# Performance work log

Hardware: AMD Instinct MI355X
Metric: run time of the kernel (lower is better)

Reference implementation:

```python
import jax, jax.numpy as jnp
import numpy as np

B, T, C, H, HS, L, V, BITS = 4, 512, 768, 12, 64, 12, 50257, 16


def _ln(x, g, b, eps=1e-5):
    m = x.mean(-1, keepdims=True)
    v = ((x - m) ** 2).mean(-1, keepdims=True)
    return (x - m) * jax.lax.rsqrt(v + eps) * g + b


def setup_inputs() -> dict:
    key = jax.random.key(0)
    ks = jax.random.split(key, 12)
    s = 0.02
    return {
        "idx": jax.random.randint(ks[0], (B, T), 0, V),
        "tok_emb": jax.random.normal(ks[1], (V, C), jnp.float32) * s,
        "pos_emb": jax.random.normal(ks[2], (T, C), jnp.float32) * s,
        "Wq": jax.random.normal(ks[3], (L, H, C, HS), jnp.float32) * s,
        "Wk": jax.random.normal(ks[4], (L, H, C, HS), jnp.float32) * s,
        "Wv": jax.random.normal(ks[5], (L, H, C, HS), jnp.float32) * s,
        "Wo": jax.random.normal(ks[6], (L, C, C), jnp.float32) * s,
        "bo": jnp.zeros((L, C), jnp.float32),
        "W1": jax.random.normal(ks[7], (L, C, 4 * C), jnp.float32) * s,
        "b1": jnp.zeros((L, 4 * C), jnp.float32),
        "W2": jax.random.normal(ks[8], (L, 4 * C, C), jnp.float32) * s,
        "b2": jnp.zeros((L, C), jnp.float32),
        "ln1_g": jnp.ones((L, C), jnp.float32),
        "ln1_b": jnp.zeros((L, C), jnp.float32),
        "ln2_g": jnp.ones((L, C), jnp.float32),
        "ln2_b": jnp.zeros((L, C), jnp.float32),
        "lnf_g": jnp.ones((C,), jnp.float32),
        "lnf_b": jnp.zeros((C,), jnp.float32),
        "Wh": jax.random.normal(ks[9], (C, BITS), jnp.float32) * s,
        "bh": jnp.zeros((BITS,), jnp.float32),
    }


def reference(idx, tok_emb, pos_emb, Wq, Wk, Wv, Wo, bo, W1, b1, W2, b2,
              ln1_g, ln1_b, ln2_g, ln2_b, lnf_g, lnf_b, Wh, bh):
    Bc, Tc = idx.shape
    x = tok_emb[idx] + pos_emb[:Tc]          # [B,T,C]
    mask = jnp.tril(jnp.ones((Tc, Tc), bool))  # causal tril buffer
    scale = HS ** -0.5

    def block(x, p):
        wq, wk, wv, wo, bo_, w1, b1_, w2, b2_, g1, bb1, g2, bb2 = p
        xn = _ln(x, g1, bb1)
        q = jnp.einsum('btc,hcd->bhtd', xn, wq)
        k = jnp.einsum('btc,hcd->bhtd', xn, wk)
        v = jnp.einsum('btc,hcd->bhtd', xn, wv)
        wei = jnp.einsum('bhtd,bhsd->bhts', q, k) * scale
        wei = jnp.where(mask, wei, -jnp.inf)
        wei = jax.nn.softmax(wei, axis=-1)
        o = jnp.einsum('bhts,bhsd->bhtd', wei, v)
        o = o.transpose(0, 2, 1, 3).reshape(Bc, Tc, H * HS)  # concat heads
        x = x + o @ wo + bo_
        xn2 = _ln(x, g2, bb2)
        h = jax.nn.gelu(xn2 @ w1 + b1_, approximate=False)  # exact GELU (torch default)
        x = x + h @ w2 + b2_
        return x, None

    x, _ = jax.lax.scan(block, x, (Wq, Wk, Wv, Wo, bo, W1, b1, W2, b2,
                                   ln1_g, ln1_b, ln2_g, ln2_b))
    x = _ln(x, lnf_g, lnf_b)
    logits = x @ Wh + bh                      # [B,T,16] ECOC logits
    return logits
```

## Files before the change

kernel.cpp:

```cpp
#include <hip/hip_runtime.h>
#include <hip/hip_bf16.h>
#include <math.h>

#define TT   512
#define CC   768
#define HH   12
#define HSZ  64
#define LL   12
#define C4   3072
#define BTOT 2048
#define NQKV 2304
#define NX   ((long)BTOT * CC)

typedef __attribute__((ext_vector_type(8))) short short8;
typedef __attribute__((ext_vector_type(4))) float f32x4;

__device__ __forceinline__ unsigned short f2b_bits(float f) {
    unsigned u = __float_as_uint(f);
    return (unsigned short)((u + 0x7fffu + ((u >> 16) & 1u)) >> 16);
}

__device__ __forceinline__ void gl_lds16(const void* g, void* l) {
    __builtin_amdgcn_global_load_lds(
        (const __attribute__((address_space(1))) unsigned int*)g,
        (__attribute__((address_space(3))) unsigned int*)l,
        16, 0, 0);
}

__global__ __launch_bounds__(256) void embed_k(const int* __restrict__ idx,
    const float* __restrict__ tok, const float* __restrict__ pos,
    float* __restrict__ x)
{
    int r   = blockIdx.x;
    int tid = threadIdx.x;
    int t   = r & (TT - 1);
    long id = idx[r];
    const float* te = tok + id * (long)CC;
    const float* pe = pos + (long)t * CC;
    float* xr = x + (long)r * CC;
#pragma unroll
    for (int i = 0; i < 3; ++i) {
        int c = tid + i * 256;
        xr[c] = te[c] + pe[c];
    }
}

__global__ __launch_bounds__(256) void ln_b(const float* __restrict__ x,
    const float* __restrict__ g, const float* __restrict__ b,
    __hip_bfloat16* __restrict__ y)
{
    int r = blockIdx.x, tid = threadIdx.x;
    const float* xr = x + (long)r * CC;
    float v[3];
    v[0] = xr[tid]; v[1] = xr[tid + 256]; v[2] = xr[tid + 512];
    float s  = v[0] + v[1] + v[2];
    float sq = v[0]*v[0] + v[1]*v[1] + v[2]*v[2];
#pragma unroll
    for (int off = 32; off > 0; off >>= 1) {
        s  += __shfl_down(s, off);
        sq += __shfl_down(sq, off);
    }
    __shared__ float ss[4], ssq[4];
    int w = tid >> 6;
    if ((tid & 63) == 0) { ss[w] = s; ssq[w] = sq; }
    __syncthreads();
    s  = ss[0] + ss[1] + ss[2] + ss[3];
    sq = ssq[0] + ssq[1] + ssq[2] + ssq[3];
    float mean = s * (1.0f / CC);
    float var  = sq * (1.0f / CC) - mean * mean;
    float rs   = rsqrtf(var + 1e-5f);
    __hip_bfloat16* yr = y + (long)r * CC;
#pragma unroll
    for (int i = 0; i < 3; ++i) {
        int c = tid + i * 256;
        yr[c] = __float2bfloat16((v[i] - mean) * rs * g[c] + b[c]);
    }
}

template <bool DOLN>
__global__ __launch_bounds__(256) void red_ln(float* __restrict__ x,
    const float* __restrict__ p, const float* __restrict__ bias,
    const float* __restrict__ g, const float* __restrict__ b,
    __hip_bfloat16* __restrict__ y)
{
    int r = blockIdx.x, tid = threadIdx.x;
    float* xr = x + (long)r * CC;
    const float* pr = p + (long)r * CC;
    float v[3];
#pragma unroll
    for (int i = 0; i < 3; ++i) {
        int c = tid + i * 256;
        float s = xr[c] + bias[c];
        s += pr[c];
        s += pr[c + 1 * NX];
        s += pr[c + 2 * NX];
        s += pr[c + 3 * NX];
        xr[c] = s;
        v[i] = s;
    }
    if (!DOLN) return;
    float s  = v[0] + v[1] + v[2];
    float sq = v[0]*v[0] + v[1]*v[1] + v[2]*v[2];
#pragma unroll
    for (int off = 32; off > 0; off >>= 1) {
        s  += __shfl_down(s, off);
        sq += __shfl_down(sq, off);
    }
    __shared__ float ss[4], ssq[4];
    int w = tid >> 6;
    if ((tid & 63) == 0) { ss[w] = s; ssq[w] = sq; }
    __syncthreads();
    s  = ss[0] + ss[1] + ss[2] + ss[3];
    sq = ssq[0] + ssq[1] + ssq[2] + ssq[3];
    float mean = s * (1.0f / CC);
    float var  = sq * (1.0f / CC) - mean * mean;
    float rs   = rsqrtf(var + 1e-5f);
    __hip_bfloat16* yr = y + (long)r * CC;
#pragma unroll
    for (int i = 0; i < 3; ++i) {
        int c = tid + i * 256;
        yr[c] = __float2bfloat16((v[i] - mean) * rs * g[c] + b[c]);
    }
}

__global__ __launch_bounds__(256) void cvtT_k(const float* __restrict__ src,
    __hip_bfloat16* __restrict__ dst, int R, int D, long sSrc, long sDst)
{
    src += (long)blockIdx.z * sSrc;
    dst += (long)blockIdx.z * sDst;
    __shared__ float t[64][65];
    int d0 = blockIdx.x * 64, r0 = blockIdx.y * 64;
    int tid = threadIdx.x;
#pragma unroll
    for (int i = 0; i < 4; ++i) {
        int flat = tid + i * 256;
        int r = flat >> 4, c4 = (flat & 15) * 4;
        float4 v = *(const float4*)&src[(long)(r0 + r) * D + d0 + c4];
        t[r][c4 + 0] = v.x; t[r][c4 + 1] = v.y;
        t[r][c4 + 2] = v.z; t[r][c4 + 3] = v.w;
    }
    __syncthreads();
#pragma unroll
    for (int i = 0; i < 4; ++i) {
        int flat = tid + i * 256;
        int n = flat >> 4, kq = (flat & 15) * 4;
        ushort4 o;
        o.x = f2b_bits(t[kq + 0][n]); o.y = f2b_bits(t[kq + 1][n]);
        o.z = f2b_bits(t[kq + 2][n]); o.w = f2b_bits(t[kq + 3][n]);
        *(ushort4*)&dst[(long)(d0 + n) * R + r0 + kq] = o;
    }
}

__global__ __launch_bounds__(256) void cvt_qkvT(const float* __restrict__ Wq,
    const float* __restrict__ Wk, const float* __restrict__ Wv,
    __hip_bfloat16* __restrict__ out)
{
    int c0 = blockIdx.x * 64;
    int g  = blockIdx.y;
    int l  = blockIdx.z;
    int which = g / 12, h = g % 12;
    const long wAtt = (long)HH * CC * HSZ;
    const float* src = (which == 0 ? Wq : which == 1 ? Wk : Wv)
                       + l * wAtt + (long)h * CC * HSZ;
    __hip_bfloat16* dst = out + (long)l * NQKV * CC + (long)(which * CC + h * HSZ) * CC;
    __shared__ float t[64][65];
    int tid = threadIdx.x;
#pragma unroll
    for (int i = 0; i < 4; ++i) {
        int flat = tid + i * 256;
        int r = flat >> 4, c4 = (flat & 15) * 4;
        float4 v = *(const float4*)&src[(long)(c0 + r) * HSZ + c4];
        t[r][c4 + 0] = v.x; t[r][c4 + 1] = v.y;
        t[r][c4 + 2] = v.z; t[r][c4 + 3] = v.w;
    }
    __syncthreads();
#pragma unroll
    for (int i = 0; i < 4; ++i) {
        int flat = tid + i * 256;
        int n = flat >> 4, kq = (flat & 15) * 4;
        ushort4 o;
        o.x = f2b_bits(t[kq + 0][n]); o.y = f2b_bits(t[kq + 1][n]);
        o.z = f2b_bits(t[kq + 2][n]); o.w = f2b_bits(t[kq + 3][n]);
        *(ushort4*)&dst[(long)n * CC + c0 + kq] = o;
    }
}

template <int EPI>
__global__ __launch_bounds__(256, 3) void gemm_bf16(
    const __hip_bfloat16* __restrict__ A,
    const __hip_bfloat16* __restrict__ BT,
    __hip_bfloat16* __restrict__ Cb, float* __restrict__ Cf,
    const float* __restrict__ bias, __hip_bfloat16* __restrict__ Vt,
    int K, int lda, int ldb, int ldc)
{
    __shared__ short Asm[4][64 * 32];
    __shared__ short Bsm[4][128 * 32];
    const int tid  = threadIdx.x;
    const int lane = tid & 63;
    const int wid  = tid >> 6;
    const int wm = wid >> 1, wn = wid & 1;
    const int row0 = blockIdx.y * 64, col0 = blockIdx.x * 128;
    const int sk = (EPI == 5) ? blockIdx.z : 0;

    const int gr = tid >> 2;
    const int cb = ((tid & 3) + (tid >> 3)) & 3;
    const int gk = cb * 8;
    const __hip_bfloat16* Ap = A  + (long)(row0 + gr) * lda + sk * K + gk;
    const __hip_bfloat16* Bp = BT + (long)(col0 + gr) * ldb + sk * K + gk;
    const int lofs = wid * 512;

    f32x4 acc[2][4] = {};
    const int fr = lane & 15, g = lane >> 4;

    int offA[2], offB[4];
#pragma unroll
    for (int m = 0; m < 2; ++m) {
        int row = wm * 32 + m * 16 + fr;
        offA[m] = row * 32 + (((g - (row >> 1)) & 3) * 8);
    }
#pragma unroll
    for (int n = 0; n < 4; ++n) {
        int row = wn * 64 + n * 16 + fr;
        offB[n] = row * 32 + (((g - (row >> 1)) & 3) * 8);
    }

#define STAGE(buf)                                                          \
    do {                                                                    \
        gl_lds16(Ap, &Asm[buf][lofs]);                                      \
        gl_lds16(Bp, &Bsm[buf][lofs]);                                      \
        gl_lds16(Bp + (long)64 * ldb, &Bsm[buf][lofs + 64 * 32]);           \
        Ap += 32; Bp += 32;                                                 \
    } while (0)

    STAGE(0); STAGE(1); STAGE(2);

    const int nt = K >> 5;
    for (int t = 0; t < nt; ++t) {
        if (t < nt - 2)       asm volatile("s_waitcnt vmcnt(6)" ::: "memory");
        else if (t == nt - 2) asm volatile("s_waitcnt vmcnt(3)" ::: "memory");
        else                  asm volatile("s_waitcnt vmcnt(0)" ::: "memory");
        __builtin_amdgcn_s_barrier();
        __builtin_amdgcn_sched_barrier(0);
        if (t + 3 < nt) STAGE((t + 3) & 3);

        const int cur = t & 3;
        short8 af[2], bf[4];
#pragma unroll
        for (int m = 0; m < 2; ++m)
            af[m] = *(const short8*)&Asm[cur][offA[m]];
#pragma unroll
        for (int n = 0; n < 4; ++n)
            bf[n] = *(const short8*)&Bsm[cur][offB[n]];
#pragma unroll
        for (int m = 0; m < 2; ++m)
#pragma unroll
            for (int n = 0; n < 4; ++n)
                acc[m][n] = __builtin_amdgcn_mfma_f32_16x16x32_bf16(
                    af[m], bf[n], acc[m][n], 0, 0, 0);
    }
#undef STAGE

    const int fq = lane >> 4;
    float* pout = (EPI == 5) ? (Cf + (long)sk * NX) : nullptr;
#pragma unroll
    for (int m = 0; m < 2; ++m) {
        int rbase = row0 + wm * 32 + m * 16 + fq * 4;
#pragma unroll
        for (int n = 0; n < 4; ++n) {
            int col = col0 + wn * 64 + n * 16 + fr;
            if (EPI == 1 && col >= 1536) {
                int hd = col - 1536;
                int b = rbase >> 9, t = rbase & (TT - 1);
                ushort4 o;
                o.x = f2b_bits(acc[m][n][0]); o.y = f2b_bits(acc[m][n][1]);
                o.z = f2b_bits(acc[m][n][2]); o.w = f2b_bits(acc[m][n][3]);
                *(ushort4*)&Vt[((long)(b * HH + (hd >> 6)) * HSZ + (hd & 63)) * TT + t] = o;
                continue;
            }
            float bv = (EPI == 2) ? bias[col] : 0.f;
#pragma unroll
            for (int j = 0; j < 4; ++j) {
                long row = rbase + j;
                float v = acc[m][n][j];
                if (EPI == 1) {
                    Cb[row * ldc + col] = __float2bfloat16(v);
                } else if (EPI == 2) {
                    v += bv;
                    v = 0.5f * v * (1.0f + erff(v * 0.70710678118654752f));
                    Cb[row * ldc + col] = __float2bfloat16(v);
                } else {
                    pout[row * ldc + col] = v;
                }
            }
        }
    }
}

__global__ __launch_bounds__(64) void attn_mfma(
    const __hip_bfloat16* __restrict__ qkv,
    const __hip_bfloat16* __restrict__ vT,
    __hip_bfloat16* __restrict__ o)
{
    const int qt = blockIdx.x;
    const int h  = blockIdx.y;
    const int b  = blockIdx.z;
    const int lane = threadIdx.x;
    const int t0 = qt * 16;
    const int fr = lane & 15, g = lane >> 4;

    __shared__ unsigned short P_lds[16 * 40];
    __shared__ float corr_lds[16], l_lds[16];

    const long qbase = ((long)(b * TT + t0 + fr)) * NQKV + h * HSZ + g * 8;
    short8 qf0 = *(const short8*)(qkv + qbase);
    short8 qf1 = *(const short8*)(qkv + qbase + 32);

    f32x4 oacc[4] = {};
    float m_run = -3.0e38f, l_run = 0.f;
    const int t_lane = t0 + fr;
    const int smax = t0 + 15;
    const long kcol = CC + h * HSZ + g * 8;
    const long vrow = (((long)(b * HH + h) * HSZ) + fr) * TT + g * 8;

    short8 ka0, ka1, ka2, ka3;
    {
        long kb0 = ((long)(b * TT + fr)) * NQKV + kcol;
        long kb1 = ((long)(b * TT + 16 + fr)) * NQKV + kcol;
        ka0 = *(const short8*)(qkv + kb0);
        ka1 = *(const short8*)(qkv + kb0 + 32);
        ka2 = *(const short8*)(qkv + kb1);
        ka3 = *(const short8*)(qkv + kb1 + 32);
    }

    for (int s0 = 0; s0 <= smax; s0 += 32) {
        f32x4 st0 = {}, st1 = {};
        st0 = __builtin_amdgcn_mfma_f32_16x16x32_bf16(ka0, qf0, st0, 0, 0, 0);
        st0 = __builtin_amdgcn_mfma_f32_16x16x32_bf16(ka1, qf1, st0, 0, 0, 0);
        st1 = __builtin_amdgcn_mfma_f32_16x16x32_bf16(ka2, qf0, st1, 0, 0, 0);
        st1 = __builtin_amdgcn_mfma_f32_16x16x32_bf16(ka3, qf1, st1, 0, 0, 0);

        const bool more = (s0 + 32 <= smax);
        short8 kn0, kn1, kn2, kn3;
        if (more) {
            long kb0 = ((long)(b * TT + s0 + 32 + fr)) * NQKV + kcol;
            long kb1 = ((long)(b * TT + s0 + 48 + fr)) * NQKV + kcol;
            kn0 = *(const short8*)(qkv + kb0);
            kn1 = *(const short8*)(qkv + kb0 + 32);
            kn2 = *(const short8*)(qkv + kb1);
            kn3 = *(const short8*)(qkv + kb1 + 32);
        }
        short8 vc0 = *(const short8*)(vT + vrow + s0);
        short8 vc1 = *(const short8*)(vT + vrow + 16 * TT + s0);
        short8 vc2 = *(const short8*)(vT + vrow + 32 * TT + s0);
        short8 vc3 = *(const short8*)(vT + vrow + 48 * TT + s0);

        float p[8];
        float mx = -3.0e38f;
#pragma unroll
        for (int j = 0; j < 4; ++j) {
            int s = s0 + g * 4 + j;
            float v = st0[j] * 0.125f;
            v = (s <= t_lane) ? v : -3.0e38f;
            p[j] = v; mx = fmaxf(mx, v);
        }
#pragma unroll
        for (int j = 0; j < 4; ++j) {
            int s = s0 + 16 + g * 4 + j;
            float v = st1[j] * 0.125f;
            v = (s <= t_lane) ? v : -3.0e38f;
            p[4 + j] = v; mx = fmaxf(mx, v);
        }
        mx = fmaxf(mx, __shfl_xor(mx, 16));
        mx = fmaxf(mx, __shfl_xor(mx, 32));
        float mnew = fmaxf(m_run, mx);
        float corr = __expf(m_run - mnew);
        float psum = 0.f;
#pragma unroll
        for (int i = 0; i < 8; ++i) {
            float e = __expf(p[i] - mnew);
            p[i] = e; psum += e;
        }
        psum += __shfl_xor(psum, 16);
        psum += __shfl_xor(psum, 32);
        l_run = l_run * corr + psum;
        m_run = mnew;

        __syncthreads();
        if (lane < 16) corr_lds[lane] = corr;
        unsigned u0 = (unsigned)f2b_bits(p[0]) | ((unsigned)f2b_bits(p[1]) << 16);
        unsigned u1 = (unsigned)f2b_bits(p[2]) | ((unsigned)f2b_bits(p[3]) << 16);
        unsigned u2 = (unsigned)f2b_bits(p[4]) | ((unsigned)f2b_bits(p[5]) << 16);
        unsigned u3 = (unsigned)f2b_bits(p[6]) | ((unsigned)f2b_bits(p[7]) << 16);
        *(unsigned*)&P_lds[fr * 40 + g * 4]          = u0;
        *(unsigned*)&P_lds[fr * 40 + g * 4 + 2]      = u1;
        *(unsigned*)&P_lds[fr * 40 + 16 + g * 4]     = u2;
        *(unsigned*)&P_lds[fr * 40 + 16 + g * 4 + 2] = u3;
        __syncthreads();

        float cr0 = corr_lds[g * 4 + 0], cr1 = corr_lds[g * 4 + 1];
        float cr2 = corr_lds[g * 4 + 2], cr3 = corr_lds[g * 4 + 3];
        short8 pf = *(const short8*)&P_lds[fr * 40 + g * 8];
        oacc[0][0] *= cr0; oacc[0][1] *= cr1; oacc[0][2] *= cr2; oacc[0][3] *= cr3;
        oacc[0] = __builtin_amdgcn_mfma_f32_16x16x32_bf16(pf, vc0, oacc[0], 0, 0, 0);
        oacc[1][0] *= cr0; oacc[1][1] *= cr1; oacc[1][2] *= cr2; oacc[1][3] *= cr3;
        oacc[1] = __builtin_amdgcn_mfma_f32_16x16x32_bf16(pf, vc1, oacc[1], 0, 0, 0);
        oacc[2][0] *= cr0; oacc[2][1] *= cr1; oacc[2][2] *= cr2; oacc[2][3] *= cr3;
        oacc[2] = __builtin_amdgcn_mfma_f32_16x16x32_bf16(pf, vc2, oacc[2], 0, 0, 0);
        oacc[3][0] *= cr0; oacc[3][1] *= cr1; oacc[3][2] *= cr2; oacc[3][3] *= cr3;
        oacc[3] = __builtin_amdgcn_mfma_f32_16x16x32_bf16(pf, vc3, oacc[3], 0, 0, 0);

        if (more) { ka0 = kn0; ka1 = kn1; ka2 = kn2; ka3 = kn3; }
    }

    __syncthreads();
    if (lane < 16) l_lds[lane] = l_run;
    __syncthreads();
    float il0 = 1.f / l_lds[g * 4 + 0], il1 = 1.f / l_lds[g * 4 + 1];
    float il2 = 1.f / l_lds[g * 4 + 2], il3 = 1.f / l_lds[g * 4 + 3];
#pragma unroll
    for (int dt = 0; dt < 4; ++dt) {
        long cbase = (long)(b * TT + t0) * CC + h * HSZ + dt * 16 + fr;
        o[cbase + (g * 4 + 0) * (long)CC] = __float2bfloat16(oacc[dt][0] * il0);
        o[cbase + (g * 4 + 1) * (long)CC] = __float2bfloat16(oacc[dt][1] * il1);
        o[cbase + (g * 4 + 2) * (long)CC] = __float2bfloat16(oacc[dt][2] * il2);
        o[cbase + (g * 4 + 3) * (long)CC] = __float2bfloat16(oacc[dt][3] * il3);
    }
}

__global__ __launch_bounds__(256) void head_k(const float* __restrict__ x,
    const float* __restrict__ g, const float* __restrict__ bb,
    const float* __restrict__ Wh, const float* __restrict__ bh,
    float* __restrict__ out)
{
    int r = blockIdx.x, tid = threadIdx.x;
    const float* xr = x + (long)r * CC;
    float v[3];
    v[0] = xr[tid]; v[1] = xr[tid + 256]; v[2] = xr[tid + 512];
    float s  = v[0] + v[1] + v[2];
    float sq = v[0]*v[0] + v[1]*v[1] + v[2]*v[2];
#pragma unroll
    for (int off = 32; off > 0; off >>= 1) {
        s  += __shfl_down(s, off);
        sq += __shfl_down(sq, off);
    }
    __shared__ float ss[4], ssq[4];
    int w = tid >> 6;
    if ((tid & 63) == 0) { ss[w] = s; ssq[w] = sq; }
    __syncthreads();
    s  = ss[0] + ss[1] + ss[2] + ss[3];
    sq = ssq[0] + ssq[1] + ssq[2] + ssq[3];
    float mean = s * (1.0f / CC);
    float var  = sq * (1.0f / CC) - mean * mean;
    float rs   = rsqrtf(var + 1e-5f);

    float acc[16];
#pragma unroll
    for (int j = 0; j < 16; ++j) acc[j] = 0.f;
#pragma unroll
    for (int i = 0; i < 3; ++i) {
        int c = tid + i * 256;
        float xnv = (v[i] - mean) * rs * g[c] + bb[c];
        const float* wr = Wh + (long)c * 16;
#pragma unroll
        for (int j = 0; j < 16; ++j) acc[j] = fmaf(xnv, wr[j], acc[j]);
    }
#pragma unroll
    for (int off = 32; off > 0; off >>= 1)
#pragma unroll
        for (int j = 0; j < 16; ++j) acc[j] += __shfl_down(acc[j], off);
    __shared__ float red[4][16];
    if ((tid & 63) == 0)
#pragma unroll
        for (int j = 0; j < 16; ++j) red[w][j] = acc[j];
    __syncthreads();
    if (tid < 16)
        out[(long)r * 16 + tid] =
            red[0][tid] + red[1][tid] + red[2][tid] + red[3][tid] + bh[tid];
}

extern "C" void kernel_launch(void* const* d_in, const int* in_sizes, int n_in,
                              void* d_out, int out_size, void* d_ws, size_t ws_size,
                              hipStream_t stream)
{
    const int*   idx  = (const int*)  d_in[0];
    const float* tok  = (const float*)d_in[1];
    const float* pos  = (const float*)d_in[2];
    const float* Wq   = (const float*)d_in[3];
    const float* Wk   = (const float*)d_in[4];
    const float* Wv   = (const float*)d_in[5];
    const float* Wo   = (const float*)d_in[6];
    const float* bo   = (const float*)d_in[7];
    const float* W1   = (const float*)d_in[8];
    const float* b1   = (const float*)d_in[9];
    const float* W2   = (const float*)d_in[10];
    const float* b2   = (const float*)d_in[11];
    const float* ln1g = (const float*)d_in[12];
    const float* ln1b = (const float*)d_in[13];
    const float* ln2g = (const float*)d_in[14];
    const float* ln2b = (const float*)d_in[15];
    const float* lnfg = (const float*)d_in[16];
    const float* lnfb = (const float*)d_in[17];
    const float* Wh   = (const float*)d_in[18];
    const float* bh   = (const float*)d_in[19];

    char* w = (char*)d_ws;
    float*          x     = (float*)w;          w += NX * 4;
    __hip_bfloat16* xn_b  = (__hip_bfloat16*)w; w += NX * 2;
    __hip_bfloat16* qkvb  = (__hip_bfloat16*)w; w += (long)BTOT * NQKV * 2;
    __hip_bfloat16* vT    = (__hip_bfloat16*)w; w += NX * 2;
    __hip_bfloat16* o_b   = (__hip_bfloat16*)w; w += NX * 2;
    __hip_bfloat16* hb    = (__hip_bfloat16*)w; w += (long)BTOT * C4 * 2;
    __hip_bfloat16* qkvT  = (__hip_bfloat16*)w; w += (long)LL * NQKV * CC * 2;
    __hip_bfloat16* woT   = (__hip_bfloat16*)w; w += (long)LL * CC * CC * 2;
    __hip_bfloat16* w1T   = (__hip_bfloat16*)w; w += (long)LL * C4 * CC * 2;
    __hip_bfloat16* w2T   = (__hip_bfloat16*)w; w += (long)LL * CC * C4 * 2;
    float*          pbuf  = (float*)w;          w += 4 * NX * 4;

    cvt_qkvT<<<dim3(12, 36, LL), 256, 0, stream>>>(Wq, Wk, Wv, qkvT);
    cvtT_k<<<dim3(12, 12, LL), 256, 0, stream>>>(Wo, woT, CC, CC,
        (long)CC * CC, (long)CC * CC);
    cvtT_k<<<dim3(48, 12, LL), 256, 0, stream>>>(W1, w1T, CC, C4,
        (long)CC * C4, (long)CC * C4);
    cvtT_k<<<dim3(12, 48, LL), 256, 0, stream>>>(W2, w2T, C4, CC,
        (long)C4 * CC, (long)C4 * CC);

    embed_k<<<BTOT, 256, 0, stream>>>(idx, tok, pos, x);
    ln_b<<<BTOT, 256, 0, stream>>>(x, ln1g, ln1b, xn_b);

    for (int l = 0; l < LL; ++l) {
        gemm_bf16<1><<<dim3(NQKV / 128, BTOT / 64), 256, 0, stream>>>(
            xn_b, qkvT + (long)l * NQKV * CC, qkvb, nullptr, nullptr, vT,
            CC, CC, CC, NQKV);

        attn_mfma<<<dim3(TT / 16, HH, 4), 64, 0, stream>>>(qkvb, vT, o_b);

        gemm_bf16<5><<<dim3(CC / 128, BTOT / 64, 4), 256, 0, stream>>>(
            o_b, woT + (long)l * CC * CC, nullptr, pbuf, nullptr, nullptr,
            192, CC, CC, CC);

        red_ln<true><<<BTOT, 256, 0, stream>>>(x, pbuf, bo + l * CC,
            ln2g + l * CC, ln2b + l * CC, xn_b);

        gemm_bf16<2><<<dim3(C4 / 128, BTOT / 64), 256, 0, stream>>>(
            xn_b, w1T + (long)l * C4 * CC, hb, nullptr, b1 + l * C4, nullptr,
            CC, CC, CC, C4);

        gemm_bf16<5><<<dim3(CC / 128, BTOT / 64, 4), 256, 0, stream>>>(
            hb, w2T + (long)l * CC * C4, nullptr, pbuf, nullptr, nullptr,
            768, C4, C4, CC);

        if (l < LL - 1) {
            red_ln<true><<<BTOT, 256, 0, stream>>>(x, pbuf, b2 + l * CC,
                ln1g + (l + 1) * CC, ln1b + (l + 1) * CC, xn_b);
        } else {
            red_ln<false><<<BTOT, 256, 0, stream>>>(x, pbuf, b2 + l * CC,
                nullptr, nullptr, nullptr);
        }
    }

    head_k<<<BTOT, 256, 0, stream>>>(x, lnfg, lnfb, Wh, bh, (float*)d_out);
}
```

Before: 1.552 ms.

## Fuse attention, output projection, residual add and LayerNorm into one kernel

```diff
diff --git a/kernel.cpp b/kernel.cpp
--- a/kernel.cpp
+++ b/kernel.cpp
@@ -296,20 +296,30 @@
     }
 }
 
-__global__ __launch_bounds__(64) void attn_mfma(
+__global__ __launch_bounds__(768) void attn_proj(
     const __hip_bfloat16* __restrict__ qkv,
     const __hip_bfloat16* __restrict__ vT,
-    __hip_bfloat16* __restrict__ o)
+    const __hip_bfloat16* __restrict__ woT,
+    const float* __restrict__ bo,
+    const float* __restrict__ g2, const float* __restrict__ bb2,
+    float* __restrict__ x, __hip_bfloat16* __restrict__ xn)
 {
     const int qt = blockIdx.x;
-    const int h  = blockIdx.y;
-    const int b  = blockIdx.z;
-    const int lane = threadIdx.x;
+    const int b  = blockIdx.y;
+    const int tid = threadIdx.x;
+    const int wid = tid >> 6;
+    const int lane = tid & 63;
+    const int h = wid;
     const int t0 = qt * 16;
     const int fr = lane & 15, g = lane >> 4;
 
-    __shared__ unsigned short P_lds[16 * 40];
-    __shared__ float corr_lds[16], l_lds[16];
+    __shared__ unsigned short o_lds[16][776];
+    __shared__ unsigned short P_all[12][16 * 40];
+    __shared__ float corr_all[12][16], l_all[12][16];
+    __shared__ float sum_w[12][16], sq_w[12][16];
+    __shared__ float mean_s[16], rs_s[16];
+
+    unsigned short* P_w = P_all[wid];
 
     const long qbase = ((long)(b * TT + t0 + fr)) * NQKV + h * HSZ + g * 8;
     short8 qf0 = *(const short8*)(qkv + qbase);
@@ -385,21 +395,20 @@
         l_run = l_run * corr + psum;
         m_run = mnew;
 
-        __syncthreads();
-        if (lane < 16) corr_lds[lane] = corr;
+        if (lane < 16) corr_all[wid][lane] = corr;
         unsigned u0 = (unsigned)f2b_bits(p[0]) | ((unsigned)f2b_bits(p[1]) << 16);
         unsigned u1 = (unsigned)f2b_bits(p[2]) | ((unsigned)f2b_bits(p[3]) << 16);
         unsigned u2 = (unsigned)f2b_bits(p[4]) | ((unsigned)f2b_bits(p[5]) << 16);
         unsigned u3 = (unsigned)f2b_bits(p[6]) | ((unsigned)f2b_bits(p[7]) << 16);
-        *(unsigned*)&P_lds[fr * 40 + g * 4]          = u0;
-        *(unsigned*)&P_lds[fr * 40 + g * 4 + 2]      = u1;
-        *(unsigned*)&P_lds[fr * 40 + 16 + g * 4]     = u2;
-        *(unsigned*)&P_lds[fr * 40 + 16 + g * 4 + 2] = u3;
-        __syncthreads();
-
-        float cr0 = corr_lds[g * 4 + 0], cr1 = corr_lds[g * 4 + 1];
-        float cr2 = corr_lds[g * 4 + 2], cr3 = corr_lds[g * 4 + 3];
-        short8 pf = *(const short8*)&P_lds[fr * 40 + g * 8];
+        *(unsigned*)&P_w[fr * 40 + g * 4]          = u0;
+        *(unsigned*)&P_w[fr * 40 + g * 4 + 2]      = u1;
+        *(unsigned*)&P_w[fr * 40 + 16 + g * 4]     = u2;
+        *(unsigned*)&P_w[fr * 40 + 16 + g * 4 + 2] = u3;
+        __builtin_amdgcn_sched_barrier(0);
+
+        float cr0 = corr_all[wid][g * 4 + 0], cr1 = corr_all[wid][g * 4 + 1];
+        float cr2 = corr_all[wid][g * 4 + 2], cr3 = corr_all[wid][g * 4 + 3];
+        short8 pf = *(const short8*)&P_w[fr * 40 + g * 8];
         oacc[0][0] *= cr0; oacc[0][1] *= cr1; oacc[0][2] *= cr2; oacc[0][3] *= cr3;
         oacc[0] = __builtin_amdgcn_mfma_f32_16x16x32_bf16(pf, vc0, oacc[0], 0, 0, 0);
         oacc[1][0] *= cr0; oacc[1][1] *= cr1; oacc[1][2] *= cr2; oacc[1][3] *= cr3;
@@ -412,18 +421,99 @@
         if (more) { ka0 = kn0; ka1 = kn1; ka2 = kn2; ka3 = kn3; }
     }
 
-    __syncthreads();
-    if (lane < 16) l_lds[lane] = l_run;
-    __syncthreads();
-    float il0 = 1.f / l_lds[g * 4 + 0], il1 = 1.f / l_lds[g * 4 + 1];
-    float il2 = 1.f / l_lds[g * 4 + 2], il3 = 1.f / l_lds[g * 4 + 3];
-#pragma unroll
-    for (int dt = 0; dt < 4; ++dt) {
-        long cbase = (long)(b * TT + t0) * CC + h * HSZ + dt * 16 + fr;
-        o[cbase + (g * 4 + 0) * (long)CC] = __float2bfloat16(oacc[dt][0] * il0);
-        o[cbase + (g * 4 + 1) * (long)CC] = __float2bfloat16(oacc[dt][1] * il1);
-        o[cbase + (g * 4 + 2) * (long)CC] = __float2bfloat16(oacc[dt][2] * il2);
-        o[cbase + (g * 4 + 3) * (long)CC] = __float2bfloat16(oacc[dt][3] * il3);
+    if (lane < 16) l_all[wid][lane] = l_run;
+    __builtin_amdgcn_sched_barrier(0);
+    {
+        float il0 = 1.f / l_all[wid][g * 4 + 0];
+        float il1 = 1.f / l_all[wid][g * 4 + 1];
+        float il2 = 1.f / l_all[wid][g * 4 + 2];
+        float il3 = 1.f / l_all[wid][g * 4 + 3];
+#pragma unroll
+        for (int dt = 0; dt < 4; ++dt) {
+            int col = h * HSZ + dt * 16 + fr;
+            o_lds[g * 4 + 0][col] = f2b_bits(oacc[dt][0] * il0);
+            o_lds[g * 4 + 1][col] = f2b_bits(oacc[dt][1] * il1);
+            o_lds[g * 4 + 2][col] = f2b_bits(oacc[dt][2] * il2);
+            o_lds[g * 4 + 3][col] = f2b_bits(oacc[dt][3] * il3);
+        }
+    }
+    __syncthreads();
+
+    const __hip_bfloat16* wb = woT + (long)(h * HSZ) * CC;
+    f32x4 pacc[4] = {};
+    short8 bc0 = *(const short8*)&wb[(0 * 16 + fr) * CC + g * 8];
+    short8 bc1 = *(const short8*)&wb[(1 * 16 + fr) * CC + g * 8];
+    short8 bc2 = *(const short8*)&wb[(2 * 16 + fr) * CC + g * 8];
+    short8 bc3 = *(const short8*)&wb[(3 * 16 + fr) * CC + g * 8];
+    for (int k0 = 0; k0 < CC; k0 += 32) {
+        short8 bn0, bn1, bn2, bn3;
+        const bool more = (k0 + 32 < CC);
+        if (more) {
+            bn0 = *(const short8*)&wb[(0 * 16 + fr) * CC + k0 + 32 + g * 8];
+            bn1 = *(const short8*)&wb[(1 * 16 + fr) * CC + k0 + 32 + g * 8];
+            bn2 = *(const short8*)&wb[(2 * 16 + fr) * CC + k0 + 32 + g * 8];
+            bn3 = *(const short8*)&wb[(3 * 16 + fr) * CC + k0 + 32 + g * 8];
+        }
+        short8 a = *(const short8*)&o_lds[fr][k0 + g * 8];
+        pacc[0] = __builtin_amdgcn_mfma_f32_16x16x32_bf16(a, bc0, pacc[0], 0, 0, 0);
+        pacc[1] = __builtin_amdgcn_mfma_f32_16x16x32_bf16(a, bc1, pacc[1], 0, 0, 0);
+        pacc[2] = __builtin_amdgcn_mfma_f32_16x16x32_bf16(a, bc2, pacc[2], 0, 0, 0);
+        pacc[3] = __builtin_amdgcn_mfma_f32_16x16x32_bf16(a, bc3, pacc[3], 0, 0, 0);
+        if (more) { bc0 = bn0; bc1 = bn1; bc2 = bn2; bc3 = bn3; }
+    }
+
+    const int fq = g;
+    float sreg[4][4];
+    float psum[4] = {}, psq[4] = {};
+#pragma unroll
+    for (int n = 0; n < 4; ++n) {
+        int col = h * HSZ + n * 16 + fr;
+        float bv = bo[col];
+#pragma unroll
+        for (int j = 0; j < 4; ++j) {
+            long R = (long)(b * TT + t0 + fq * 4 + j);
+            float s = x[R * CC + col] + pacc[n][j] + bv;
+            x[R * CC + col] = s;
+            sreg[n][j] = s;
+            psum[j] += s; psq[j] += s * s;
+        }
+    }
+#pragma unroll
+    for (int mk = 1; mk < 16; mk <<= 1) {
+#pragma unroll
+        for (int j = 0; j < 4; ++j) {
+            psum[j] += __shfl_xor(psum[j], mk);
+            psq[j]  += __shfl_xor(psq[j], mk);
+        }
+    }
+    if (fr == 0) {
+#pragma unroll
+        for (int j = 0; j < 4; ++j) {
+            sum_w[wid][fq * 4 + j] = psum[j];
+            sq_w[wid][fq * 4 + j]  = psq[j];
+        }
+    }
+    __syncthreads();
+    if (tid < 16) {
+        float S = 0.f, Q = 0.f;
+#pragma unroll
+        for (int w = 0; w < 12; ++w) { S += sum_w[w][tid]; Q += sq_w[w][tid]; }
+        float mean = S * (1.0f / CC);
+        float var  = Q * (1.0f / CC) - mean * mean;
+        mean_s[tid] = mean;
+        rs_s[tid]   = rsqrtf(var + 1e-5f);
+    }
+    __syncthreads();
+#pragma unroll
+    for (int n = 0; n < 4; ++n) {
+        int col = h * HSZ + n * 16 + fr;
+#pragma unroll
+        for (int j = 0; j < 4; ++j) {
+            int r = fq * 4 + j;
+            long R = (long)(b * TT + t0 + r);
+            xn[R * CC + col] = __float2bfloat16(
+                (sreg[n][j] - mean_s[r]) * rs_s[r] * g2[col] + bb2[col]);
+        }
     }
 }
 
@@ -508,7 +598,6 @@
     __hip_bfloat16* xn_b  = (__hip_bfloat16*)w; w += NX * 2;
     __hip_bfloat16* qkvb  = (__hip_bfloat16*)w; w += (long)BTOT * NQKV * 2;
     __hip_bfloat16* vT    = (__hip_bfloat16*)w; w += NX * 2;
-    __hip_bfloat16* o_b   = (__hip_bfloat16*)w; w += NX * 2;
     __hip_bfloat16* hb    = (__hip_bfloat16*)w; w += (long)BTOT * C4 * 2;
     __hip_bfloat16* qkvT  = (__hip_bfloat16*)w; w += (long)LL * NQKV * CC * 2;
     __hip_bfloat16* woT   = (__hip_bfloat16*)w; w += (long)LL * CC * CC * 2;
@@ -532,14 +621,9 @@
             xn_b, qkvT + (long)l * NQKV * CC, qkvb, nullptr, nullptr, vT,
             CC, CC, CC, NQKV);
 
-        attn_mfma<<<dim3(TT / 16, HH, 4), 64, 0, stream>>>(qkvb, vT, o_b);
-
-        gemm_bf16<5><<<dim3(CC / 128, BTOT / 64, 4), 256, 0, stream>>>(
-            o_b, woT + (long)l * CC * CC, nullptr, pbuf, nullptr, nullptr,
-            192, CC, CC, CC);
-
-        red_ln<true><<<BTOT, 256, 0, stream>>>(x, pbuf, bo + l * CC,
-            ln2g + l * CC, ln2b + l * CC, xn_b);
+        attn_proj<<<dim3(TT / 16, 4), 768, 0, stream>>>(
+            qkvb, vT, woT + (long)l * CC * CC, bo + l * CC,
+            ln2g + l * CC, ln2b + l * CC, x, xn_b);
 
         gemm_bf16<2><<<dim3(C4 / 128, BTOT / 64), 256, 0, stream>>>(
             xn_b, w1T + (long)l * C4 * CC, hb, nullptr, b1 + l * C4, nullptr,
```

Result: slower. 1.992 ms (+28.3%).
